# Kernel tuning notes

Hardware: AMD Instinct MI355X
Metric: run time of the kernel (lower is better)

Reference implementation:

```python
import jax, jax.numpy as jnp
import numpy as np

W = 8        # detection window (hard-coded in original forward)
ALPHA = 0.5  # mixing weight (hard-coded in original forward)


def setup_inputs() -> dict:
    key = jax.random.key(0)
    k1, k2 = jax.random.split(key)
    B, T = 8192, 2048
    outputs = jax.random.uniform(k1, (B, T), dtype=jnp.float32)
    labels = jax.random.randint(k2, (B, T), 0, 2)
    return {"outputs": outputs, "labels": labels}


def _dd2_prefix(p, L):
    """Vectorized loss_delay_detection_2 on the prefix p[:, :L] per row.
    p: [B, T] probs, L: [B] int prefix lengths (0 allowed -> loss 0)."""
    B, T = p.shape
    k = jnp.arange(T)
    mask = k[None, :] < L[:, None]                       # [B, T]
    p_eff = jnp.where(mask, p, 0.0)
    # prod[0] = 1, prod[k] = 1 - p[k-1]
    prodv = 1.0 - jnp.pad(p_eff[:, :-1], ((0, 0), (1, 0)))
    cp = jnp.cumprod(prodv, axis=1)                       # [B, T]
    terms = (k + 1).astype(p.dtype)[None, :] * p_eff * cp
    return jnp.sum(jnp.where(mask, terms, 0.0), axis=1)   # [B]


def reference(outputs, labels):
    B, T = outputs.shape
    diff = labels != labels[:, :1]
    has_change = jnp.any(diff, axis=1)                    # [B]
    ind0 = jnp.argmax(diff, axis=1)                       # [B], 0 if no change

    # --- false-alarm part: 1 - dd2 over full row (no change) or prefix [:ind0]
    L_fa = jnp.where(has_change, ind0, T)
    fa = 1.0 - _dd2_prefix(outputs, L_fa)                 # [B]

    # --- delay-detection part on window outputs[i, ind0:ind0+W] (torch truncates at T)
    kw = jnp.arange(W)
    idx = ind0[:, None] + kw[None, :]                     # [B, W]
    valid = idx < T                                       # k < n
    p_win = jnp.take_along_axis(outputs, jnp.clip(idx, 0, T - 1), axis=1)
    p_win = jnp.where(valid, p_win, 0.0)
    n = jnp.minimum(W, T - ind0)                          # window length, >= 1
    prodv = 1.0 - jnp.pad(p_win[:, :-1], ((0, 0), (1, 0)))
    cp = jnp.cumprod(prodv, axis=1)                       # [B, W]
    term1 = jnp.sum(
        jnp.where(valid, (kw + 1).astype(outputs.dtype)[None, :] * p_win * cp, 0.0),
        axis=1,
    )
    # torch.prod(prod[1:]) == cumprod[n-1]; scalar term broadcast over n elems -> * n
    cp_last = jnp.take_along_axis(cp, (n - 1)[:, None], axis=1)[:, 0]
    p_last = jnp.take_along_axis(p_win, (n - 1)[:, None], axis=1)[:, 0]
    dd = term1 + n.astype(outputs.dtype) * (W + 1) * cp_last * (1.0 - p_last)

    per_sample = jnp.where(has_change, ALPHA * dd + (1.0 - ALPHA) * fa, fa)
    return jnp.mean(per_sample)
```

## Files before the change

kernel.cpp:

```cpp
#include <hip/hip_runtime.h>

#define TLEN 2048
#define BROWS 8192
#define W 8

__global__ __launch_bounds__(256) void
custom_loss_kernel(const float* __restrict__ outputs,
                   const int* __restrict__ labels,
                   float* __restrict__ out) {
    const int wave = threadIdx.x >> 6;
    const int lane = threadIdx.x & 63;
    const int row  = blockIdx.x * 4 + wave;

    const float* __restrict__ orow = outputs + (size_t)row * TLEN;
    const int*   __restrict__ lrow = labels  + (size_t)row * TLEN;

    const int lab0 = lrow[0];
    int ind0 = -1;
    for (int base = 0; base < TLEN; base += 64) {
        int lab = lrow[base + lane];
        unsigned long long m = __ballot(lab != lab0);
        if (m) { ind0 = base + __ffsll(m) - 1; break; }
    }
    const bool has_change = (ind0 >= 0);
    const int L = has_change ? ind0 : TLEN;

    float S = 0.0f;
    float carry = 1.0f;
    for (int base = 0; base < L && carry != 0.0f; base += 64) {
        const int k = base + lane;
        const bool act = (k < L);
        const float p = act ? orow[k] : 0.0f;
        float incl = act ? (1.0f - p) : 1.0f;
        #pragma unroll
        for (int off = 1; off < 64; off <<= 1) {
            float o = __shfl_up(incl, off, 64);
            if (lane >= off) incl *= o;
        }
        float excl = __shfl_up(incl, 1, 64);
        if (lane == 0) excl = 1.0f;
        float term = act ? ((float)(k + 1) * p * carry * excl) : 0.0f;
        #pragma unroll
        for (int off = 32; off; off >>= 1) term += __shfl_xor(term, off, 64);
        S += term;
        carry *= __shfl(incl, 63, 64);
    }
    const float fa = 1.0f - S;

    float per_sample = fa;
    if (has_change) {
        float pw = 0.0f;
        const int idx = ind0 + lane;
        if (lane < W && idx < TLEN) pw = orow[idx];
        const int n = min(W, TLEN - ind0);
        float cp = 1.0f, term1 = 0.0f, cpl = 1.0f, pl = 0.0f;
        #pragma unroll
        for (int k = 0; k < W; ++k) {
            if (k < n) {
                float pk = __shfl(pw, k, 64);
                term1 += (float)(k + 1) * pk * cp;
                cpl = cp; pl = pk;
                cp *= (1.0f - pk);
            }
        }
        const float dd = term1 + (float)n * (float)(W + 1) * cpl * (1.0f - pl);
        per_sample = 0.5f * dd + 0.5f * fa;
    }

    __shared__ float sred[4];
    if (lane == 0) sred[wave] = per_sample;
    __syncthreads();
    if (threadIdx.x == 0) {
        float s = sred[0] + sred[1] + sred[2] + sred[3];
        atomicAdd(out, s * (1.0f / (float)BROWS));
    }
}

extern "C" void kernel_launch(void* const* d_in, const int* in_sizes, int n_in,
                              void* d_out, int out_size, void* d_ws, size_t ws_size,
                              hipStream_t stream) {
    const float* outputs = (const float*)d_in[0];
    const int*   labels  = (const int*)d_in[1];
    float* out = (float*)d_out;

    hipMemsetAsync(out, 0, sizeof(float), stream);

    custom_loss_kernel<<<BROWS / 4, 256, 0, stream>>>(outputs, labels, out);
}
```

Measured before the change: 145.4 us.

## Add single-chunk fast path and replace atomic accumulation with two-stage reduction

Adds a fast path for rows whose first label change and detection window lie inside the first 64 elements. It computes both loss parts from a single coalesced load of labels and probabilities, using wave shuffles instead of extra dependent global loads. Other rows fall back to the original chunked scan. The memset plus per-block atomicAdd is replaced by per-block partials written to workspace and a separate single-block reduction kernel, which adds one extra launch.

```diff
diff --git a/kernel.cpp b/kernel.cpp
--- a/kernel.cpp
+++ b/kernel.cpp
@@ -3,11 +3,12 @@
 #define TLEN 2048
 #define BROWS 8192
 #define W 8
+#define NBLK (BROWS / 4)
 
 __global__ __launch_bounds__(256) void
-custom_loss_kernel(const float* __restrict__ outputs,
-                   const int* __restrict__ labels,
-                   float* __restrict__ out) {
+loss_rows_kernel(const float* __restrict__ outputs,
+                 const int* __restrict__ labels,
+                 float* __restrict__ partials) {
     const int wave = threadIdx.x >> 6;
     const int lane = threadIdx.x & 63;
     const int row  = blockIdx.x * 4 + wave;
@@ -15,22 +16,19 @@
     const float* __restrict__ orow = outputs + (size_t)row * TLEN;
     const int*   __restrict__ lrow = labels  + (size_t)row * TLEN;
 
-    const int lab0 = lrow[0];
-    int ind0 = -1;
-    for (int base = 0; base < TLEN; base += 64) {
-        int lab = lrow[base + lane];
-        unsigned long long m = __ballot(lab != lab0);
-        if (m) { ind0 = base + __ffsll(m) - 1; break; }
-    }
-    const bool has_change = (ind0 >= 0);
-    const int L = has_change ? ind0 : TLEN;
+    const int   lab = lrow[lane];
+    const float p   = orow[lane];
 
-    float S = 0.0f;
-    float carry = 1.0f;
-    for (int base = 0; base < L && carry != 0.0f; base += 64) {
-        const int k = base + lane;
-        const bool act = (k < L);
-        const float p = act ? orow[k] : 0.0f;
+    const int lab0 = __shfl(lab, 0, 64);
+    const unsigned long long m0 = __ballot(lab != lab0);
+    const int ind0f = m0 ? (__ffsll(m0) - 1) : -1;
+
+    float per_sample;
+
+    if (m0 && ind0f + W <= 64) {
+        const int ind0 = ind0f;
+        const bool act = lane < ind0;
+        const float pe = act ? p : 0.0f;
         float incl = act ? (1.0f - p) : 1.0f;
         #pragma unroll
         for (int off = 1; off < 64; off <<= 1) {
@@ -39,41 +37,93 @@
         }
         float excl = __shfl_up(incl, 1, 64);
         if (lane == 0) excl = 1.0f;
-        float term = act ? ((float)(k + 1) * p * carry * excl) : 0.0f;
+        float term = (float)(lane + 1) * pe * excl;
         #pragma unroll
         for (int off = 32; off; off >>= 1) term += __shfl_xor(term, off, 64);
-        S += term;
-        carry *= __shfl(incl, 63, 64);
-    }
-    const float fa = 1.0f - S;
+        const float fa = 1.0f - term;
 
-    float per_sample = fa;
-    if (has_change) {
-        float pw = 0.0f;
-        const int idx = ind0 + lane;
-        if (lane < W && idx < TLEN) pw = orow[idx];
-        const int n = min(W, TLEN - ind0);
         float cp = 1.0f, term1 = 0.0f, cpl = 1.0f, pl = 0.0f;
         #pragma unroll
         for (int k = 0; k < W; ++k) {
-            if (k < n) {
-                float pk = __shfl(pw, k, 64);
-                term1 += (float)(k + 1) * pk * cp;
-                cpl = cp; pl = pk;
-                cp *= (1.0f - pk);
+            float pk = __shfl(p, ind0 + k, 64);
+            term1 += (float)(k + 1) * pk * cp;
+            cpl = cp; pl = pk;
+            cp *= (1.0f - pk);
+        }
+        const float dd = term1 + (float)W * (float)(W + 1) * cpl * (1.0f - pl);
+        per_sample = 0.5f * (dd + fa);
+    } else {
+        int ind0 = -1;
+        for (int base = 0; base < TLEN; base += 64) {
+            int lb = (base == 0) ? lab : lrow[base + lane];
+            unsigned long long m = __ballot(lb != lab0);
+            if (m) { ind0 = base + __ffsll(m) - 1; break; }
+        }
+        const bool has_change = (ind0 >= 0);
+        const int L = has_change ? ind0 : TLEN;
+
+        float S = 0.0f, carry = 1.0f;
+        for (int base = 0; base < L && carry != 0.0f; base += 64) {
+            const int k = base + lane;
+            const bool act = (k < L);
+            const float pk = act ? orow[k] : 0.0f;
+            float incl = act ? (1.0f - pk) : 1.0f;
+            #pragma unroll
+            for (int off = 1; off < 64; off <<= 1) {
+                float o = __shfl_up(incl, off, 64);
+                if (lane >= off) incl *= o;
             }
+            float excl = __shfl_up(incl, 1, 64);
+            if (lane == 0) excl = 1.0f;
+            float term = act ? ((float)(k + 1) * pk * carry * excl) : 0.0f;
+            #pragma unroll
+            for (int off = 32; off; off >>= 1) term += __shfl_xor(term, off, 64);
+            S += term;
+            carry *= __shfl(incl, 63, 64);
         }
-        const float dd = term1 + (float)n * (float)(W + 1) * cpl * (1.0f - pl);
-        per_sample = 0.5f * dd + 0.5f * fa;
+        const float fa = 1.0f - S;
+
+        per_sample = fa;
+        if (has_change) {
+            float pw = 0.0f;
+            const int idx = ind0 + lane;
+            if (lane < W && idx < TLEN) pw = orow[idx];
+            const int n = min(W, TLEN - ind0);
+            float cp = 1.0f, term1 = 0.0f, cpl = 1.0f, pl = 0.0f;
+            #pragma unroll
+            for (int k = 0; k < W; ++k) {
+                if (k < n) {
+                    float pk = __shfl(pw, k, 64);
+                    term1 += (float)(k + 1) * pk * cp;
+                    cpl = cp; pl = pk;
+                    cp *= (1.0f - pk);
+                }
+            }
+            const float dd = term1 + (float)n * (float)(W + 1) * cpl * (1.0f - pl);
+            per_sample = 0.5f * dd + 0.5f * fa;
+        }
     }
 
     __shared__ float sred[4];
     if (lane == 0) sred[wave] = per_sample;
     __syncthreads();
-    if (threadIdx.x == 0) {
-        float s = sred[0] + sred[1] + sred[2] + sred[3];
-        atomicAdd(out, s * (1.0f / (float)BROWS));
-    }
+    if (threadIdx.x == 0)
+        partials[blockIdx.x] = sred[0] + sred[1] + sred[2] + sred[3];
+}
+
+__global__ __launch_bounds__(256) void
+loss_reduce_kernel(const float* __restrict__ partials,
+                   float* __restrict__ out) {
+    const int tid = threadIdx.x;
+    float s = 0.0f;
+    #pragma unroll
+    for (int i = 0; i < NBLK / 256; ++i) s += partials[tid + i * 256];
+    #pragma unroll
+    for (int off = 32; off; off >>= 1) s += __shfl_xor(s, off, 64);
+    __shared__ float sr[4];
+    if ((tid & 63) == 0) sr[tid >> 6] = s;
+    __syncthreads();
+    if (tid == 0) out[0] = (sr[0] + sr[1] + sr[2] + sr[3]) * (1.0f / (float)BROWS);
 }
 
 extern "C" void kernel_launch(void* const* d_in, const int* in_sizes, int n_in,
@@ -81,9 +131,9 @@
                               hipStream_t stream) {
     const float* outputs = (const float*)d_in[0];
     const int*   labels  = (const int*)d_in[1];
-    float* out = (float*)d_out;
+    float* out      = (float*)d_out;
+    float* partials = (float*)d_ws;
 
-    hipMemsetAsync(out, 0, sizeof(float), stream);
-
-    custom_loss_kernel<<<BROWS / 4, 256, 0, stream>>>(outputs, labels, out);
+    loss_rows_kernel<<<NBLK, 256, 0, stream>>>(outputs, labels, partials);
+    loss_reduce_kernel<<<1, 256, 0, stream>>>(partials, out);
 }
```

New measurement: 120.6 us (median of 2 runs). -17.1%, faster.
